# Optimization experiments

Hardware: AMD Instinct MI355X
Metric: run time of the kernel (lower is better)

Reference implementation:

```python
import jax, jax.numpy as jnp
import numpy as np

B, D, K = 32768, 256, 1024


def setup_inputs() -> dict:
    key = jax.random.key(0)
    k1, k2 = jax.random.split(key)
    embedding = jax.random.normal(k1, (B, D), dtype=jnp.float32)
    codebook = jax.random.normal(k2, (K, D), dtype=jnp.float32)
    return {"embedding": embedding, "codebook": codebook}


def reference(embedding, codebook):
    # code_norms: (K,) squared L2 norm of each code
    code_norms = jnp.sum(codebook ** 2, axis=1)            # (K,)
    dots = embedding @ codebook.T                           # (B, K)
    alpha = dots / code_norms[None, :]                      # (B, K)
    # error for projecting e onto line of code c:
    #   ||e - alpha c||^2 = ||e||^2 - dots^2 / ||c||^2
    # (identical math to materializing (B,K,D) diff, without the blowup)
    e_norms = jnp.sum(embedding ** 2, axis=1, keepdims=True)  # (B, 1)
    errors = e_norms - dots ** 2 / code_norms[None, :]        # (B, K)
    indices = jnp.argmin(errors, axis=1)                      # (B,)
    # gather chosen projection: alpha[b, idx[b]] * codebook[idx[b]]
    alpha_sel = jnp.take_along_axis(alpha, indices[:, None], axis=1)  # (B, 1)
    z_out = alpha_sel * codebook[indices]                     # (B, D)
    return (z_out, indices)
```

## Files before the change

kernel.cpp:

```cpp
#include <hip/hip_runtime.h>
#include <cstdint>

#define B_ROWS 32768
#define DIM    256
#define KCODES 1024

typedef _Float16 f16x8 __attribute__((ext_vector_type(8)));
typedef float    f32x4 __attribute__((ext_vector_type(4)));


__global__ __launch_bounds__(64) void vq_prep(const float* __restrict__ cb,
                                              _Float16* __restrict__ hi,
                                              _Float16* __restrict__ lo,
                                              float* __restrict__ inv_norm) {
  const int k = blockIdx.x;
  const int lane = threadIdx.x;
  float4 c = reinterpret_cast<const float4*>(cb)[k * 64 + lane];
  float nrm = c.x * c.x + c.y * c.y + c.z * c.z + c.w * c.w;
#pragma unroll
  for (int off = 32; off; off >>= 1) nrm += __shfl_xor(nrm, off);
  if (lane == 0) inv_norm[k] = 1.0f / nrm;

  float f[4] = {c.x, c.y, c.z, c.w};
  _Float16 h[4], l[4];
#pragma unroll
  for (int i = 0; i < 4; ++i) {
    h[i] = (_Float16)f[i];
    l[i] = (_Float16)((f[i] - (float)h[i]) * 2048.0f);
  }
  const int phys = (lane >> 1) ^ (k & 15);
  const int byteoff = k * 512 + phys * 16 + (lane & 1) * 8;
  *reinterpret_cast<uint2*>((char*)hi + byteoff) = *reinterpret_cast<uint2*>(h);
  *reinterpret_cast<uint2*>((char*)lo + byteoff) = *reinterpret_cast<uint2*>(l);
}

__device__ __forceinline__ void gld16(const void* g, void* l) {
  __builtin_amdgcn_global_load_lds(
      (const __attribute__((address_space(1))) uint32_t*)g,
      (__attribute__((address_space(3))) uint32_t*)l, 16, 0, 0);
}

__global__ __launch_bounds__(256, 1) void vq_main(const float* __restrict__ emb,
                                                  const float* __restrict__ cb,
                                                  const _Float16* __restrict__ cbh,
                                                  const _Float16* __restrict__ cbl,
                                                  const float* __restrict__ inv_g,
                                                  float* __restrict__ out) {
  __shared__ uint4 Btile[2][1024];
  __shared__ float inv_s[KCODES];
  __shared__ int   sk[128];
  __shared__ float sd[128];

  const int flat = threadIdx.x;
  const int wave = flat >> 6;
  const int lane = flat & 63;
  const int quad = lane >> 4;
  const int lr   = lane & 15;

  reinterpret_cast<float4*>(inv_s)[flat] = reinterpret_cast<const float4*>(inv_g)[flat];

  f16x8 Ah[2][8], Al[2][8];
  const int row0 = blockIdx.x * 128 + wave * 32;
#pragma unroll
  for (int s = 0; s < 2; ++s) {
    const float* rp = emb + (size_t)(row0 + s * 16 + lr) * DIM;
#pragma unroll
    for (int c = 0; c < 8; ++c) {
      const float* p = rp + c * 32 + quad * 8;
      float4 f0 = *reinterpret_cast<const float4*>(p);
      float4 f1 = *reinterpret_cast<const float4*>(p + 4);
      float f[8] = {f0.x, f0.y, f0.z, f0.w, f1.x, f1.y, f1.z, f1.w};
      f16x8 h, l;
#pragma unroll
      for (int j = 0; j < 8; ++j) {
        _Float16 hv = (_Float16)f[j];
        h[j] = hv;
        l[j] = (_Float16)((f[j] - (float)hv) * 2048.0f);
      }
      Ah[s][c] = h;
      Al[s][c] = l;
    }
  }

  auto stage = [&](int buf, int t) {
    const char* srcH = (const char*)cbh + t * 8192;
    const char* srcL = (const char*)cbl + t * 8192;
    char* dst = (char*)&Btile[buf][0];
    const int off = flat * 16;
    gld16(srcH + off,        dst + off);
    gld16(srcH + 4096 + off, dst + 4096 + off);
    gld16(srcL + off,        dst + 8192 + off);
    gld16(srcL + 4096 + off, dst + 12288 + off);
  };
  stage(0, 0);

  float bg[2][4], bd[2][4];
  int   bk[2][4];
#pragma unroll
  for (int s = 0; s < 2; ++s)
#pragma unroll
    for (int r = 0; r < 4; ++r) { bg[s][r] = -1.0f; bd[s][r] = 0.0f; bk[s][r] = 0; }

  for (int t = 0; t < 64; ++t) {
    __syncthreads();
    if (t + 1 < 64) stage((t + 1) & 1, t + 1);
    const char* buf = (const char*)&Btile[t & 1][0];

    f32x4 accA0 = {0, 0, 0, 0}, accB0 = {0, 0, 0, 0};
    f32x4 accA1 = {0, 0, 0, 0}, accB1 = {0, 0, 0, 0};
#pragma unroll
    for (int c = 0; c < 8; ++c) {
      const int g = (((c * 4 + quad) ^ lr) * 16) + lr * 512;
      f16x8 bh = *reinterpret_cast<const f16x8*>(buf + g);
      f16x8 bl = *reinterpret_cast<const f16x8*>(buf + 8192 + g);
      accA0 = __builtin_amdgcn_mfma_f32_16x16x32_f16(Ah[0][c], bh, accA0, 0, 0, 0);
      accA1 = __builtin_amdgcn_mfma_f32_16x16x32_f16(Ah[1][c], bh, accA1, 0, 0, 0);
      accB0 = __builtin_amdgcn_mfma_f32_16x16x32_f16(Al[0][c], bh, accB0, 0, 0, 0);
      accB1 = __builtin_amdgcn_mfma_f32_16x16x32_f16(Al[1][c], bh, accB1, 0, 0, 0);
      accB0 = __builtin_amdgcn_mfma_f32_16x16x32_f16(Ah[0][c], bl, accB0, 0, 0, 0);
      accB1 = __builtin_amdgcn_mfma_f32_16x16x32_f16(Ah[1][c], bl, accB1, 0, 0, 0);
    }

    const int n = t * 16 + lr;
    const float inl = inv_s[n];
#pragma unroll
    for (int r = 0; r < 4; ++r) {
      float d0 = accA0[r] + accB0[r] * 4.8828125e-4f;
      float g0 = d0 * d0 * inl;
      if (g0 > bg[0][r]) { bg[0][r] = g0; bd[0][r] = d0; bk[0][r] = n; }
      float d1 = accA1[r] + accB1[r] * 4.8828125e-4f;
      float g1 = d1 * d1 * inl;
      if (g1 > bg[1][r]) { bg[1][r] = g1; bd[1][r] = d1; bk[1][r] = n; }
    }
  }

#pragma unroll
  for (int s = 0; s < 2; ++s) {
#pragma unroll
    for (int r = 0; r < 4; ++r) {
      float g = bg[s][r]; int k = bk[s][r]; float d = bd[s][r];
#pragma unroll
      for (int m = 1; m < 16; m <<= 1) {
        float g2 = __shfl_xor(g, m);
        int   k2 = __shfl_xor(k, m);
        float d2 = __shfl_xor(d, m);
        if (g2 > g || (g2 == g && k2 < k)) { g = g2; k = k2; d = d2; }
      }
      if (lr == 0) {
        const int row = wave * 32 + s * 16 + quad * 4 + r;
        sk[row] = k;
        sd[row] = d;
      }
    }
  }
  __syncthreads();

  const int orow = blockIdx.x * 128;
#pragma unroll 4
  for (int i = 0; i < 32; ++i) {
    const int row = i * 4 + wave;
    const int k = sk[row];
    const float alpha = sd[row] * inv_s[k];
    float4 c4 = reinterpret_cast<const float4*>(cb)[k * 64 + lane];
    float4 z = {alpha * c4.x, alpha * c4.y, alpha * c4.z, alpha * c4.w};
    reinterpret_cast<float4*>(out)[(size_t)(orow + row) * 64 + lane] = z;
  }
  if (flat < 128) {
    out[(size_t)B_ROWS * DIM + orow + flat] = (float)sk[flat];
  }
}

extern "C" void kernel_launch(void* const* d_in, const int* in_sizes, int n_in,
                              void* d_out, int out_size, void* d_ws, size_t ws_size,
                              hipStream_t stream) {
  const float* emb = (const float*)d_in[0];
  const float* cb  = (const float*)d_in[1];
  _Float16* cbh = (_Float16*)d_ws;
  _Float16* cbl = (_Float16*)((char*)d_ws + (512 << 10));
  float*    inv = (float*)((char*)d_ws + (1 << 20));

  vq_prep<<<KCODES, 64, 0, stream>>>(cb, cbh, cbl, inv);
  vq_main<<<B_ROWS / 128, 256, 0, stream>>>(emb, cb, cbh, cbl, inv, (float*)d_out);
}
```

Measured before the change: 158.2 us.

## Split codebook across blocks and add separate argmin reduce kernel

The codebook scan is divided into four splits, so each block handles a quarter of the codes for its 128 rows. This raises the grid from 256 to 1024 blocks, and the launch bound now permits 4 blocks per CU. Each split writes a per-row candidate (dot, index) to workspace. A new reduce kernel combines the candidates and gathers the scaled codebook row. The extra parallelism and occupancy come at the cost of re-reading and re-converting the embedding once per split, plus an extra launch and candidate traffic.

```diff
diff --git a/kernel.cpp b/kernel.cpp
--- a/kernel.cpp
+++ b/kernel.cpp
@@ -4,6 +4,7 @@
 #define B_ROWS 32768
 #define DIM    256
 #define KCODES 1024
+#define NSPLIT 4
 
 typedef _Float16 f16x8 __attribute__((ext_vector_type(8)));
 typedef float    f32x4 __attribute__((ext_vector_type(4)));
@@ -40,16 +41,13 @@
       (__attribute__((address_space(3))) uint32_t*)l, 16, 0, 0);
 }
 
-__global__ __launch_bounds__(256, 1) void vq_main(const float* __restrict__ emb,
-                                                  const float* __restrict__ cb,
+__global__ __launch_bounds__(256, 4) void vq_main(const float* __restrict__ emb,
                                                   const _Float16* __restrict__ cbh,
                                                   const _Float16* __restrict__ cbl,
                                                   const float* __restrict__ inv_g,
-                                                  float* __restrict__ out) {
+                                                  float2* __restrict__ cand) {
   __shared__ uint4 Btile[2][1024];
   __shared__ float inv_s[KCODES];
-  __shared__ int   sk[128];
-  __shared__ float sd[128];
 
   const int flat = threadIdx.x;
   const int wave = flat >> 6;
@@ -57,10 +55,14 @@
   const int quad = lane >> 4;
   const int lr   = lane & 15;
 
+  const int split  = blockIdx.x & (NSPLIT - 1);
+  const int rowblk = blockIdx.x >> 2;
+  const int t0 = split * 16;
+
   reinterpret_cast<float4*>(inv_s)[flat] = reinterpret_cast<const float4*>(inv_g)[flat];
 
   f16x8 Ah[2][8], Al[2][8];
-  const int row0 = blockIdx.x * 128 + wave * 32;
+  const int row0 = rowblk * 128 + wave * 32;
 #pragma unroll
   for (int s = 0; s < 2; ++s) {
     const float* rp = emb + (size_t)(row0 + s * 16 + lr) * DIM;
@@ -92,18 +94,18 @@
     gld16(srcL + off,        dst + 8192 + off);
     gld16(srcL + 4096 + off, dst + 12288 + off);
   };
-  stage(0, 0);
+  stage(0, t0);
 
   float bg[2][4], bd[2][4];
   int   bk[2][4];
 #pragma unroll
   for (int s = 0; s < 2; ++s)
 #pragma unroll
-    for (int r = 0; r < 4; ++r) { bg[s][r] = -1.0f; bd[s][r] = 0.0f; bk[s][r] = 0; }
+    for (int r = 0; r < 4; ++r) { bg[s][r] = -1.0f; bd[s][r] = 0.0f; bk[s][r] = t0 * 16; }
 
-  for (int t = 0; t < 64; ++t) {
+  for (int t = t0; t < t0 + 16; ++t) {
     __syncthreads();
-    if (t + 1 < 64) stage((t + 1) & 1, t + 1);
+    if (t + 1 < t0 + 16) stage((t + 1) & 1, t + 1);
     const char* buf = (const char*)&Btile[t & 1][0];
 
     f32x4 accA0 = {0, 0, 0, 0}, accB0 = {0, 0, 0, 0};
@@ -147,27 +149,37 @@
         if (g2 > g || (g2 == g && k2 < k)) { g = g2; k = k2; d = d2; }
       }
       if (lr == 0) {
-        const int row = wave * 32 + s * 16 + quad * 4 + r;
-        sk[row] = k;
-        sd[row] = d;
+        const int row = row0 + s * 16 + quad * 4 + r;
+        cand[(size_t)split * B_ROWS + row] = make_float2(d, __int_as_float(k));
       }
     }
   }
-  __syncthreads();
+}
 
-  const int orow = blockIdx.x * 128;
-#pragma unroll 4
-  for (int i = 0; i < 32; ++i) {
-    const int row = i * 4 + wave;
-    const int k = sk[row];
-    const float alpha = sd[row] * inv_s[k];
-    float4 c4 = reinterpret_cast<const float4*>(cb)[k * 64 + lane];
-    float4 z = {alpha * c4.x, alpha * c4.y, alpha * c4.z, alpha * c4.w};
-    reinterpret_cast<float4*>(out)[(size_t)(orow + row) * 64 + lane] = z;
+__global__ __launch_bounds__(256) void vq_reduce(const float2* __restrict__ cand,
+                                                 const float* __restrict__ inv_g,
+                                                 const float* __restrict__ cb,
+                                                 float* __restrict__ out) {
+  const int wave = threadIdx.x >> 6;
+  const int lane = threadIdx.x & 63;
+  const int row = blockIdx.x * 4 + wave;
+
+  float best_g = -1.0f, best_d = 0.0f;
+  int best_k = 0;
+#pragma unroll
+  for (int s = 0; s < NSPLIT; ++s) {
+    float2 c = cand[(size_t)s * B_ROWS + row];
+    int k = __float_as_int(c.y);
+    float g = c.x * c.x * inv_g[k];
+    if (g > best_g || (g == best_g && k < best_k)) {
+      best_g = g; best_d = c.x; best_k = k;
+    }
   }
-  if (flat < 128) {
-    out[(size_t)B_ROWS * DIM + orow + flat] = (float)sk[flat];
-  }
+  const float alpha = best_d * inv_g[best_k];
+  float4 c4 = reinterpret_cast<const float4*>(cb)[best_k * 64 + lane];
+  float4 z = {alpha * c4.x, alpha * c4.y, alpha * c4.z, alpha * c4.w};
+  reinterpret_cast<float4*>(out)[(size_t)row * 64 + lane] = z;
+  if (lane == 0) out[(size_t)B_ROWS * DIM + row] = (float)best_k;
 }
 
 extern "C" void kernel_launch(void* const* d_in, const int* in_sizes, int n_in,
@@ -178,7 +190,9 @@
   _Float16* cbh = (_Float16*)d_ws;
   _Float16* cbl = (_Float16*)((char*)d_ws + (512 << 10));
   float*    inv = (float*)((char*)d_ws + (1 << 20));
+  float2*   cand = (float2*)((char*)d_ws + (1 << 20) + 4096);
 
   vq_prep<<<KCODES, 64, 0, stream>>>(cb, cbh, cbl, inv);
-  vq_main<<<B_ROWS / 128, 256, 0, stream>>>(emb, cb, cbh, cbl, inv, (float*)d_out);
+  vq_main<<<(B_ROWS / 128) * NSPLIT, 256, 0, stream>>>(emb, cbh, cbl, inv, cand);
+  vq_reduce<<<B_ROWS / 4, 256, 0, stream>>>(cand, inv, cb, (float*)d_out);
 }
```

Result: slower. 289.9 us (+83.3%).
